# Optimization experiments

Hardware: AMD Instinct MI355X
Metric: run time of the kernel (lower is better)

## Reference

```python
import jax, jax.numpy as jnp
import numpy as np

F32 = jnp.float32
FP8_MAX = 448.0          # E4M3 max normal
MIN_NORM_EXP = -6.0      # smallest normal exponent for E4M3 (bias 7)


def _floor_log2(a):
    """Exact floor(log2(a)) for a>0 (with correction for fp rounding); 0 -> 0."""
    a_safe = jnp.where(a > 0, a, 1.0)
    e = jnp.floor(jnp.log2(a_safe))
    p = jnp.exp2(e)
    e = jnp.where(a_safe >= 2.0 * p, e + 1.0, jnp.where(a_safe < p, e - 1.0, e))
    return jax.lax.stop_gradient(e)


def quant_e4m3(x):
    """Round-to-nearest-even quantization to FP8 E4M3 (saturating, no NaN)."""
    a = jnp.abs(x)
    e = jnp.maximum(_floor_log2(a), MIN_NORM_EXP)
    step = jnp.exp2(e - 3.0)                 # mantissa ULP (3 mantissa bits)
    q = jnp.round(a / step) * step           # jnp.round = round-half-even
    q = jnp.minimum(q, FP8_MAX)
    q = jnp.where(a > 0, q, 0.0)
    return jnp.where(x < 0, -q, q)


def bits_to_float(b):
    """Decode [..., 8] spike bits (sign, e3..e0, m2..m0) to float32 E4M3 value."""
    sign = 1.0 - 2.0 * b[..., 0]
    exp = b[..., 1] * 8.0 + b[..., 2] * 4.0 + b[..., 3] * 2.0 + b[..., 4]
    man = b[..., 5] * 4.0 + b[..., 6] * 2.0 + b[..., 7]
    mag = jnp.where(exp > 0,
                    (1.0 + man / 8.0) * jnp.exp2(exp - 7.0),   # normal
                    (man / 8.0) * jnp.exp2(MIN_NORM_EXP))       # subnormal
    return sign * mag


def float_to_bits(x):
    """Encode an FP8-representable float32 into [..., 8] spike bits."""
    sgn = (x < 0).astype(F32)
    a = jnp.abs(x)
    e = jnp.clip(_floor_log2(a), MIN_NORM_EXP, 8.0)
    is_norm = a >= jnp.exp2(MIN_NORM_EXP)
    ef = jnp.where(is_norm, e + 7.0, 0.0)
    man = jnp.where(is_norm, a * jnp.exp2(-e) * 8.0 - 8.0, a * jnp.exp2(9.0))
    man = jnp.clip(jnp.round(man), 0.0, 7.0)

    def bit(v, k):
        return jnp.floor(v / (2.0 ** k)) % 2.0

    return jnp.stack([sgn,
                      bit(ef, 3), bit(ef, 2), bit(ef, 1), bit(ef, 0),
                      bit(man, 2), bit(man, 1), bit(man, 0)], axis=-1)


B, IN, OUT = 256, 512, 1024


def setup_inputs() -> dict:
    key = jax.random.key(0)
    kx, kw = jax.random.split(key)
    # random floats -> quantize to FP8 -> encode as spike bits (valid pulses)
    x_f = jax.random.normal(kx, (B, IN), F32)
    w_f = jax.random.normal(kw, (OUT, IN), F32) * (1.0 / 32.0)  # keep accum < 448
    x = float_to_bits(quant_e4m3(x_f))                 # [B, IN, 8]
    weight_pulse = float_to_bits(quant_e4m3(w_f))      # [OUT, IN, 8]
    return {"x": x, "weight_pulse": weight_pulse}


def reference(x, weight_pulse):
    # SpikeFP8Linear_Fast, mode='sequential':
    # products[i] = fp8(x_i * w_i); acc = fp8(...fp8(p0 + p1) + ... + p_{N-1})
    xf = bits_to_float(x)             # [B, IN]
    wf = bits_to_float(weight_pulse)  # [OUT, IN]

    p0 = quant_e4m3(xf[:, 0][:, None] * wf[None, :, 0])  # [B, OUT]
    xs = jnp.moveaxis(xf[:, 1:], 1, 0)  # [IN-1, B]
    ws = jnp.moveaxis(wf[:, 1:], 1, 0)  # [IN-1, OUT]

    def step(acc, xw):
        xi, wi = xw
        p = quant_e4m3(xi[:, None] * wi[None, :])
        return quant_e4m3(acc + p), None

    acc, _ = jax.lax.scan(step, p0, (xs, ws))
    return float_to_bits(acc)  # [B, OUT, 8]
```

## Files before the change

kernel.cpp:

```cpp
#include <hip/hip_runtime.h>

#define B_DIM 256
#define IN_DIM 512
#define OUT_DIM 1024

typedef __attribute__((__ext_vector_type__(2))) float v2f;

__device__ __forceinline__ float dec_pair(float4 a, float4 b) {
    int ef  = ((int)a.y << 3) | ((int)a.z << 2) | ((int)a.w << 1) | (int)b.x;
    int man = ((int)b.y << 2) | ((int)b.z << 1) | (int)b.w;
    float mag;
    if (ef > 0)
        mag = __uint_as_float(((unsigned)(ef + 120) << 23) | ((unsigned)man << 20));
    else
        mag = (float)man * 0.001953125f;
    return (a.x != 0.0f) ? -mag : mag;
}

__global__ void k_decode(const float* __restrict__ xbits,
                         const float* __restrict__ wbits,
                         float* __restrict__ xf, float* __restrict__ wt) {
    int v = blockIdx.x * 256 + threadIdx.x;
    if (v < B_DIM * IN_DIM) {
        const float4* p = (const float4*)xbits + (size_t)v * 2;
        xf[v] = dec_pair(p[0], p[1]);
    } else {
        int u = v - B_DIM * IN_DIM;
        const float4* p = (const float4*)wbits + (size_t)u * 2;
        float val = dec_pair(p[0], p[1]);
        int o = u >> 9, i = u & 511;
        wt[((size_t)(i >> 2) * OUT_DIM + o) * 4 + (i & 3)] = val;
    }
}

__device__ __forceinline__ void store8(float* __restrict__ out, int idx, float v) {
    unsigned au = __float_as_uint(v) & 0x7fffffffu;
    float sgn = (v < 0.0f) ? 1.0f : 0.0f;
    int ef, man;
    if (au >= 0x3c800000u) {
        ef  = (int)(au >> 23) - 120;
        man = (int)((au >> 20) & 7u);
    } else {
        ef  = 0;
        man = (int)(__uint_as_float(au) * 512.0f);
    }
    float4 lo = make_float4(sgn,
                            (float)((ef >> 3) & 1), (float)((ef >> 2) & 1),
                            (float)((ef >> 1) & 1));
    float4 hi = make_float4((float)(ef & 1),
                            (float)((man >> 2) & 1), (float)((man >> 1) & 1),
                            (float)(man & 1));
    float4* op = (float4*)(out + (size_t)idx * 8);
    op[0] = lo;
    op[1] = hi;
}

__device__ __forceinline__ v2f qpk(v2f v) {
    int q = __builtin_amdgcn_cvt_pk_fp8_f32(v.x, v.y, 0, false);
    return __builtin_amdgcn_cvt_pk_f32_fp8(q, false);
}

__device__ __forceinline__ v2f qprod(v2f xp, float wk) {
    v2f wv = {wk, wk};
    return qpk(xp * wv);
}

__global__ __launch_bounds__(256) void k_main(const float* __restrict__ xf,
                                              const float* __restrict__ wt,
                                              float* __restrict__ out) {
    __shared__ float xs[8 * IN_DIM];
    int tid  = threadIdx.x;
    int lane = tid & 63;
    int wid  = tid >> 6;
    int o  = blockIdx.x * 64 + lane;
    int b0 = blockIdx.y * 8 + wid * 2;

    {
        const float4* ra = (const float4*)(xf + (size_t)b0 * IN_DIM) + lane * 2;
        const float4* rb = (const float4*)(xf + (size_t)(b0 + 1) * IN_DIM) + lane * 2;
        float4 a0 = ra[0], a1 = ra[1];
        float4 c0 = rb[0], c1 = rb[1];
        float4* dst = (float4*)(xs + (size_t)wid * 2 * IN_DIM) + lane * 4;
        dst[0] = make_float4(a0.x, c0.x, a0.y, c0.y);
        dst[1] = make_float4(a0.z, c0.z, a0.w, c0.w);
        dst[2] = make_float4(a1.x, c1.x, a1.y, c1.y);
        dst[3] = make_float4(a1.z, c1.z, a1.w, c1.w);
    }
    __syncthreads();

    const float4* xls = (const float4*)(xs + (size_t)wid * 2 * IN_DIM);
    const float4* wq  = (const float4*)wt + o;

    v2f acc = {0.0f, 0.0f};

#pragma unroll
    for (int g = 0; g < 64; ++g) {
        float4 x0 = xls[4 * g + 0];
        float4 x1 = xls[4 * g + 1];
        float4 x2 = xls[4 * g + 2];
        float4 x3 = xls[4 * g + 3];
        float4 wa = wq[(size_t)(2 * g + 0) * OUT_DIM];
        float4 wb = wq[(size_t)(2 * g + 1) * OUT_DIM];
        const v2f* xp0 = (const v2f*)&x0;
        const v2f* xp1 = (const v2f*)&x1;
        const v2f* xp2 = (const v2f*)&x2;
        const v2f* xp3 = (const v2f*)&x3;
        v2f p0 = qprod(xp0[0], wa.x);
        v2f p1 = qprod(xp0[1], wa.y);
        v2f p2 = qprod(xp1[0], wa.z);
        v2f p3 = qprod(xp1[1], wa.w);
        v2f p4 = qprod(xp2[0], wb.x);
        v2f p5 = qprod(xp2[1], wb.y);
        v2f p6 = qprod(xp3[0], wb.z);
        v2f p7 = qprod(xp3[1], wb.w);
        acc = qpk(acc + p0);
        acc = qpk(acc + p1);
        acc = qpk(acc + p2);
        acc = qpk(acc + p3);
        acc = qpk(acc + p4);
        acc = qpk(acc + p5);
        acc = qpk(acc + p6);
        acc = qpk(acc + p7);
    }

    store8(out, b0 * OUT_DIM + o, acc.x);
    store8(out, (b0 + 1) * OUT_DIM + o, acc.y);
}

extern "C" void kernel_launch(void* const* d_in, const int* in_sizes, int n_in,
                              void* d_out, int out_size, void* d_ws, size_t ws_size,
                              hipStream_t stream) {
    const float* xb = (const float*)d_in[0];
    const float* wb = (const float*)d_in[1];
    float* out = (float*)d_out;

    float* xf = (float*)d_ws;
    float* wt = (float*)d_ws + B_DIM * IN_DIM;

    int total = B_DIM * IN_DIM + OUT_DIM * IN_DIM;
    k_decode<<<dim3(total / 256), dim3(256), 0, stream>>>(xb, wb, xf, wt);

    dim3 grid(OUT_DIM / 64, B_DIM / 8);
    k_main<<<grid, dim3(256), 0, stream>>>(xf, wt, out);
}
```

Measured before the change: 96.54 us.

## Fuse bit decoding into main kernel with packed FP8 bytes in LDS

Drops the separate decode kernel and its float workspace. Each 512-thread block now decodes its own 64-output weight slice and 16 batch rows straight from the spike-bit inputs into packed FP8 bytes in shared memory, using XOR-swizzled weight storage. The inner loop unpacks operands with hardware fp8-to-f32 conversions, cutting one launch and the workspace round trip. The cost is that every block re-reads large weight and activation bit tensors from global memory, so the bit data is read many times over instead of once.

```diff
diff --git a/kernel.cpp b/kernel.cpp
--- a/kernel.cpp
+++ b/kernel.cpp
@@ -6,31 +6,13 @@
 
 typedef __attribute__((__ext_vector_type__(2))) float v2f;
 
-__device__ __forceinline__ float dec_pair(float4 a, float4 b) {
-    int ef  = ((int)a.y << 3) | ((int)a.z << 2) | ((int)a.w << 1) | (int)b.x;
-    int man = ((int)b.y << 2) | ((int)b.z << 1) | (int)b.w;
-    float mag;
-    if (ef > 0)
-        mag = __uint_as_float(((unsigned)(ef + 120) << 23) | ((unsigned)man << 20));
-    else
-        mag = (float)man * 0.001953125f;
-    return (a.x != 0.0f) ? -mag : mag;
+__device__ __forceinline__ unsigned bit_of(float f) {
+    return (__float_as_uint(f) >> 23) & 1u;
 }
-
-__global__ void k_decode(const float* __restrict__ xbits,
-                         const float* __restrict__ wbits,
-                         float* __restrict__ xf, float* __restrict__ wt) {
-    int v = blockIdx.x * 256 + threadIdx.x;
-    if (v < B_DIM * IN_DIM) {
-        const float4* p = (const float4*)xbits + (size_t)v * 2;
-        xf[v] = dec_pair(p[0], p[1]);
-    } else {
-        int u = v - B_DIM * IN_DIM;
-        const float4* p = (const float4*)wbits + (size_t)u * 2;
-        float val = dec_pair(p[0], p[1]);
-        int o = u >> 9, i = u & 511;
-        wt[((size_t)(i >> 2) * OUT_DIM + o) * 4 + (i & 3)] = val;
-    }
+__device__ __forceinline__ unsigned byte_of(float4 a, float4 b) {
+    return (bit_of(a.x) << 7) | (bit_of(a.y) << 6) | (bit_of(a.z) << 5) |
+           (bit_of(a.w) << 4) | (bit_of(b.x) << 3) | (bit_of(b.y) << 2) |
+           (bit_of(b.z) << 1) |  bit_of(b.w);
 }
 
 __device__ __forceinline__ void store8(float* __restrict__ out, int idx, float v) {
@@ -60,71 +42,70 @@
     return __builtin_amdgcn_cvt_pk_f32_fp8(q, false);
 }
 
-__device__ __forceinline__ v2f qprod(v2f xp, float wk) {
-    v2f wv = {wk, wk};
-    return qpk(xp * wv);
-}
+__global__ __launch_bounds__(512) void k_fused(const float* __restrict__ xbits,
+                                               const float* __restrict__ wbits,
+                                               float* __restrict__ out) {
+    __shared__ unsigned       wq4[128 * 64];
+    __shared__ unsigned short xp [512 * 8];
 
-__global__ __launch_bounds__(256) void k_main(const float* __restrict__ xf,
-                                              const float* __restrict__ wt,
-                                              float* __restrict__ out) {
-    __shared__ float xs[8 * IN_DIM];
     int tid  = threadIdx.x;
     int lane = tid & 63;
-    int wid  = tid >> 6;
-    int o  = blockIdx.x * 64 + lane;
-    int b0 = blockIdx.y * 8 + wid * 2;
+    int w    = tid >> 6;
+    int bid  = blockIdx.x;
+    int s    = bid & 15;
+    int grp  = bid >> 4;
 
-    {
-        const float4* ra = (const float4*)(xf + (size_t)b0 * IN_DIM) + lane * 2;
-        const float4* rb = (const float4*)(xf + (size_t)(b0 + 1) * IN_DIM) + lane * 2;
-        float4 a0 = ra[0], a1 = ra[1];
-        float4 c0 = rb[0], c1 = rb[1];
-        float4* dst = (float4*)(xs + (size_t)wid * 2 * IN_DIM) + lane * 4;
-        dst[0] = make_float4(a0.x, c0.x, a0.y, c0.y);
-        dst[1] = make_float4(a0.z, c0.z, a0.w, c0.w);
-        dst[2] = make_float4(a1.x, c1.x, a1.y, c1.y);
-        dst[3] = make_float4(a1.z, c1.z, a1.w, c1.w);
+    for (int c = 0; c < 16; ++c) {
+        int q   = c * 512 + tid;
+        int o_l = q >> 7;
+        int i4  = q & 127;
+        const float4* p = (const float4*)(wbits +
+            ((size_t)(s * 64 + o_l) * IN_DIM + i4 * 4) * 8);
+        unsigned b0 = byte_of(p[0], p[1]);
+        unsigned b1 = byte_of(p[2], p[3]);
+        unsigned b2 = byte_of(p[4], p[5]);
+        unsigned b3 = byte_of(p[6], p[7]);
+        wq4[i4 * 64 + (o_l ^ (i4 & 63))] = b0 | (b1 << 8) | (b2 << 16) | (b3 << 24);
+    }
+    for (int c = 0; c < 16; ++c) {
+        const float4* p = (const float4*)(xbits +
+            ((size_t)(grp * 16 + c) * IN_DIM + tid) * 8);
+        unsigned by = byte_of(p[0], p[1]);
+        ((unsigned char*)xp)[tid * 16 + c] = (unsigned char)by;
     }
     __syncthreads();
 
-    const float4* xls = (const float4*)(xs + (size_t)wid * 2 * IN_DIM);
-    const float4* wq  = (const float4*)wt + o;
-
+    int og = s * 64 + lane;
+    const unsigned short* xw = xp + w;
     v2f acc = {0.0f, 0.0f};
 
-#pragma unroll
-    for (int g = 0; g < 64; ++g) {
-        float4 x0 = xls[4 * g + 0];
-        float4 x1 = xls[4 * g + 1];
-        float4 x2 = xls[4 * g + 2];
-        float4 x3 = xls[4 * g + 3];
-        float4 wa = wq[(size_t)(2 * g + 0) * OUT_DIM];
-        float4 wb = wq[(size_t)(2 * g + 1) * OUT_DIM];
-        const v2f* xp0 = (const v2f*)&x0;
-        const v2f* xp1 = (const v2f*)&x1;
-        const v2f* xp2 = (const v2f*)&x2;
-        const v2f* xp3 = (const v2f*)&x3;
-        v2f p0 = qprod(xp0[0], wa.x);
-        v2f p1 = qprod(xp0[1], wa.y);
-        v2f p2 = qprod(xp1[0], wa.z);
-        v2f p3 = qprod(xp1[1], wa.w);
-        v2f p4 = qprod(xp2[0], wb.x);
-        v2f p5 = qprod(xp2[1], wb.y);
-        v2f p6 = qprod(xp3[0], wb.z);
-        v2f p7 = qprod(xp3[1], wb.w);
-        acc = qpk(acc + p0);
-        acc = qpk(acc + p1);
-        acc = qpk(acc + p2);
-        acc = qpk(acc + p3);
-        acc = qpk(acc + p4);
-        acc = qpk(acc + p5);
-        acc = qpk(acc + p6);
-        acc = qpk(acc + p7);
+#pragma unroll 4
+    for (int i4 = 0; i4 < 128; ++i4) {
+        unsigned wq = wq4[i4 * 64 + (lane ^ (i4 & 63))];
+        v2f w01 = __builtin_amdgcn_cvt_pk_f32_fp8((int)wq, false);
+        v2f w23 = __builtin_amdgcn_cvt_pk_f32_fp8((int)wq, true);
+        int ib = i4 * 4;
+        {
+            v2f xv = __builtin_amdgcn_cvt_pk_f32_fp8((int)xw[(ib + 0) * 8], false);
+            acc = qpk(acc + qpk(xv * (v2f){w01.x, w01.x}));
+        }
+        {
+            v2f xv = __builtin_amdgcn_cvt_pk_f32_fp8((int)xw[(ib + 1) * 8], false);
+            acc = qpk(acc + qpk(xv * (v2f){w01.y, w01.y}));
+        }
+        {
+            v2f xv = __builtin_amdgcn_cvt_pk_f32_fp8((int)xw[(ib + 2) * 8], false);
+            acc = qpk(acc + qpk(xv * (v2f){w23.x, w23.x}));
+        }
+        {
+            v2f xv = __builtin_amdgcn_cvt_pk_f32_fp8((int)xw[(ib + 3) * 8], false);
+            acc = qpk(acc + qpk(xv * (v2f){w23.y, w23.y}));
+        }
     }
 
-    store8(out, b0 * OUT_DIM + o, acc.x);
-    store8(out, (b0 + 1) * OUT_DIM + o, acc.y);
+    int b0 = grp * 16 + 2 * w;
+    store8(out, b0 * OUT_DIM + og, acc.x);
+    store8(out, (b0 + 1) * OUT_DIM + og, acc.y);
 }
 
 extern "C" void kernel_launch(void* const* d_in, const int* in_sizes, int n_in,
@@ -133,13 +114,7 @@
     const float* xb = (const float*)d_in[0];
     const float* wb = (const float*)d_in[1];
     float* out = (float*)d_out;
+    (void)d_ws; (void)ws_size;
 
-    float* xf = (float*)d_ws;
-    float* wt = (float*)d_ws + B_DIM * IN_DIM;
-
-    int total = B_DIM * IN_DIM + OUT_DIM * IN_DIM;
-    k_decode<<<dim3(total / 256), dim3(256), 0, stream>>>(xb, wb, xf, wt);
-
-    dim3 grid(OUT_DIM / 64, B_DIM / 8);
-    k_main<<<grid, dim3(256), 0, stream>>>(xf, wt, out);
+    k_fused<<<dim3(256), dim3(512), 0, stream>>>(xb, wb, out);
 }
```

After: 126.9 us. 31.4% more time.
